# Performance work log

Hardware: AMD Instinct MI355X
Metric: run time of the kernel (lower is better)

The kernel has to match this reference:

```python
import jax, jax.numpy as jnp
import numpy as np

B, L, D, H = 64, 1024, 256, 256


def setup_inputs() -> dict:
    key = jax.random.key(0)
    ks = jax.random.split(key, 10)
    s = 0.05  # small init to keep tanh/sigmoid in linear-ish range
    return {
        "x":  jax.random.normal(ks[0], (B, L, D), jnp.float32),
        # LSTM cell params (keras gate order i, f, g, o)
        "Wk": jax.random.normal(ks[1], (D, 4 * H), jnp.float32) * s,
        "Wr": jax.random.normal(ks[2], (H, 4 * H), jnp.float32) * s,
        "b":  jnp.zeros((4 * H,), jnp.float32),
        # Attention params
        "W1": jax.random.normal(ks[3], (D, H), jnp.float32) * s,
        "b1": jnp.zeros((H,), jnp.float32),
        "W2": jax.random.normal(ks[4], (H, H), jnp.float32) * s,
        "b2": jnp.zeros((H,), jnp.float32),
        "V":  jax.random.normal(ks[5], (H, 1), jnp.float32) * s,
        "bV": jnp.zeros((1,), jnp.float32),
    }


def reference(x, Wk, Wr, b, W1, b1, W2, b2, V, bV):
    Bb, Ll, Dd = x.shape
    Hh = Wr.shape[0]
    # Encoder projection, computed once (W1 @ encoder_outputs)
    w1_e = jnp.einsum('bld,dh->blh', x, W1) + b1            # (B, L, H)
    # Decoder input is the last encoder step, repeated every step
    x_in = x[:, -1, :]                                      # (B, D)
    xz = x_in @ Wk + b                                      # (B, 4H), constant per step
    h0 = jnp.zeros((Bb, Hh), x.dtype)
    c0 = jnp.zeros((Bb, Hh), x.dtype)

    def step(carry, _):
        h, c = carry
        z = xz + h @ Wr                                     # (B, 4H)
        i, f, g, o = jnp.split(z, 4, axis=-1)
        i = jax.nn.sigmoid(i)
        f = jax.nn.sigmoid(f)
        g = jnp.tanh(g)
        o = jax.nn.sigmoid(o)
        c = f * c + i * g
        h = o * jnp.tanh(c)
        # Additive (Bahdanau) attention: v^T tanh(W1 e + W2 d)
        w2_d = (h @ W2 + b2)[:, None, :]                    # (B, 1, H)
        scores = jnp.tanh(w1_e + w2_d) @ V + bV             # (B, L, 1)
        attn = jax.nn.softmax(scores[..., 0], axis=1)       # (B, L)
        return (h, c), attn

    _, attn_seq = jax.lax.scan(step, (h0, c0), None, length=Ll)  # (L, B, L)
    return jnp.transpose(attn_seq, (1, 0, 2))               # (B, L_steps, L_ptr)
```

## Files before the change

kernel.cpp:

```cpp
#include <hip/hip_runtime.h>
#include <hip/hip_bf16.h>


#define LOG2E  1.4426950408889634f
#define C2LOG2E 2.8853900817779268f

typedef float f32x2 __attribute__((ext_vector_type(2)));

__device__ __forceinline__ unsigned f2bf(float f) {
  unsigned u = __builtin_bit_cast(unsigned, f);
  return (u + 0x7fffu + ((u >> 16) & 1u)) >> 16;
}
__device__ __forceinline__ float bfbits2f(unsigned bits) {
  return __builtin_bit_cast(float, bits << 16);
}
__device__ __forceinline__ float bfhi2f(unsigned bits) {
  return __builtin_bit_cast(float, bits & 0xffff0000u);
}

#define CHEAP_BAR()                                            \
  do {                                                         \
    asm volatile("s_waitcnt lgkmcnt(0)\n\ts_barrier" ::: "memory"); \
    __builtin_amdgcn_sched_barrier(0);                         \
  } while (0)

#if defined(__has_builtin)
#  if __has_builtin(__builtin_amdgcn_fdot2_f32_bf16)
#    define HAS_DOT2_BF16 1
#  endif
#endif

#if defined(HAS_DOT2_BF16)
typedef __bf16 bf16x2v __attribute__((ext_vector_type(2)));
__device__ __forceinline__ float dot2bf(unsigned w, unsigned h, float acc) {
  return __builtin_amdgcn_fdot2_f32_bf16(__builtin_bit_cast(bf16x2v, w),
                                         __builtin_bit_cast(bf16x2v, h), acc, false);
}
#else
__device__ __forceinline__ float dot2bf(unsigned w, unsigned h, float acc) {
  float wl = __builtin_bit_cast(float, w << 16);
  float wh = __builtin_bit_cast(float, w & 0xffff0000u);
  float hl = __builtin_bit_cast(float, h << 16);
  float hh = __builtin_bit_cast(float, h & 0xffff0000u);
  return fmaf(wh, hh, fmaf(wl, hl, acc));
}
#endif

#if defined(__has_builtin) && __has_builtin(__builtin_amdgcn_rcpf)
#  define FAST_RCP(x) __builtin_amdgcn_rcpf(x)
#else
#  define FAST_RCP(x) (1.0f / (x))
#endif

__device__ __forceinline__ float fast_sigmoid(float x) {
  return FAST_RCP(1.f + exp2f(-LOG2E * x));
}
__device__ __forceinline__ float fast_tanh(float x) {
  return 1.f - 2.f * FAST_RCP(1.f + exp2f(C2LOG2E * x));
}

__global__ __launch_bounds__(256) void k2_xz(const float* __restrict__ x,
                                             const float* __restrict__ Wk,
                                             const float* __restrict__ bvec,
                                             float* __restrict__ xz) {
  const int b = blockIdx.x, tid = threadIdx.x;
  float acc[4] = {bvec[tid], bvec[256 + tid], bvec[512 + tid], bvec[768 + tid]};
  const float* xr = x + ((size_t)b * 1024 + 1023) * 256;
  for (int d0 = 0; d0 < 256; d0 += 4) {
    const float4 xv = *(const float4*)(xr + d0);
#pragma unroll
    for (int i = 0; i < 4; ++i) {
      const float xs = (i == 0) ? xv.x : (i == 1) ? xv.y : (i == 2) ? xv.z : xv.w;
#pragma unroll
      for (int q = 0; q < 4; ++q)
        acc[q] = fmaf(xs, Wk[(size_t)(d0 + i) * 1024 + q * 256 + tid], acc[q]);
    }
  }
#pragma unroll
  for (int q = 0; q < 4; ++q) xz[b * 1024 + q * 256 + tid] = acc[q];
}

__global__
__attribute__((amdgpu_flat_work_group_size(512, 512), amdgpu_waves_per_eu(2, 2)))
void k3_fat(const float* __restrict__ xz,
            const float* __restrict__ Wr,
            unsigned short* __restrict__ hseq,
            const float* __restrict__ x,
            const float* __restrict__ W1,
            const float* __restrict__ b1,
            uint2* __restrict__ ATq) {
  __shared__ __align__(16) unsigned smem[8 * 1024 * 4 + 512 + 128];
  const int tid = threadIdx.x;
  if (blockIdx.x < 64) {
    unsigned* Wtail = smem;
    float*    z_lds = (float*)(smem + 32768);
    unsigned* h_pk  = smem + 32768 + 512;
    const int b = blockIdx.x;
    const int colA = tid, colB = tid + 512;

    unsigned wA[96], wB[96];
#pragma unroll
    for (int p = 0; p < 96; ++p) {
      wA[p] = f2bf(Wr[(size_t)(2 * p) * 1024 + colA]) |
              (f2bf(Wr[(size_t)(2 * p + 1) * 1024 + colA]) << 16);
      wB[p] = f2bf(Wr[(size_t)(2 * p) * 1024 + colB]) |
              (f2bf(Wr[(size_t)(2 * p + 1) * 1024 + colB]) << 16);
    }
#pragma unroll
    for (int gg = 0; gg < 8; ++gg) {
#pragma unroll
      for (int d = 0; d < 4; ++d) {
        const int p = 96 + gg * 4 + d;
        Wtail[(gg * 1024 + colA) * 4 + d] =
            f2bf(Wr[(size_t)(2 * p) * 1024 + colA]) |
            (f2bf(Wr[(size_t)(2 * p + 1) * 1024 + colA]) << 16);
        Wtail[(gg * 1024 + colB) * 4 + d] =
            f2bf(Wr[(size_t)(2 * p) * 1024 + colB]) |
            (f2bf(Wr[(size_t)(2 * p + 1) * 1024 + colB]) << 16);
      }
    }
    if (tid < 128) h_pk[tid] = 0u;
    const float zaA = xz[b * 1024 + colA];
    const float zaB = xz[b * 1024 + colB];
    float c = 0.f;
    CHEAP_BAR();

    for (int t = 0; t < 1024; ++t) {
      float aA0 = zaA, aA1 = 0.f, aB0 = zaB, aB1 = 0.f;
#pragma unroll
      for (int g = 0; g < 12; ++g) {
        const uint4 hp = *(const uint4*)&h_pk[4 * g];
        aA0 = dot2bf(wA[4 * g + 0], hp.x, aA0);
        aA0 = dot2bf(wA[4 * g + 1], hp.y, aA0);
        aA0 = dot2bf(wA[4 * g + 2], hp.z, aA0);
        aA0 = dot2bf(wA[4 * g + 3], hp.w, aA0);
        aB0 = dot2bf(wB[4 * g + 0], hp.x, aB0);
        aB0 = dot2bf(wB[4 * g + 1], hp.y, aB0);
        aB0 = dot2bf(wB[4 * g + 2], hp.z, aB0);
        aB0 = dot2bf(wB[4 * g + 3], hp.w, aB0);
      }
#pragma unroll
      for (int g = 12; g < 24; ++g) {
        const uint4 hp = *(const uint4*)&h_pk[4 * g];
        aA1 = dot2bf(wA[4 * g + 0], hp.x, aA1);
        aA1 = dot2bf(wA[4 * g + 1], hp.y, aA1);
        aA1 = dot2bf(wA[4 * g + 2], hp.z, aA1);
        aA1 = dot2bf(wA[4 * g + 3], hp.w, aA1);
        aB1 = dot2bf(wB[4 * g + 0], hp.x, aB1);
        aB1 = dot2bf(wB[4 * g + 1], hp.y, aB1);
        aB1 = dot2bf(wB[4 * g + 2], hp.z, aB1);
        aB1 = dot2bf(wB[4 * g + 3], hp.w, aB1);
      }
#pragma unroll
      for (int gg = 0; gg < 8; ++gg) {
        const uint4 hp = *(const uint4*)&h_pk[96 + 4 * gg];
        const uint4 wa = *(const uint4*)&Wtail[(gg * 1024 + colA) * 4];
        const uint4 wb = *(const uint4*)&Wtail[(gg * 1024 + colB) * 4];
        float& rA = (gg < 4) ? aA0 : aA1;
        float& rB = (gg < 4) ? aB0 : aB1;
        rA = dot2bf(wa.x, hp.x, rA);
        rA = dot2bf(wa.y, hp.y, rA);
        rA = dot2bf(wa.z, hp.z, rA);
        rA = dot2bf(wa.w, hp.w, rA);
        rB = dot2bf(wb.x, hp.x, rB);
        rB = dot2bf(wb.y, hp.y, rB);
        rB = dot2bf(wb.z, hp.z, rB);
        rB = dot2bf(wb.w, hp.w, rB);
      }
      const float aA = aA0 + aA1;
      const float aB = aB0 + aB1;
      if (tid >= 256) {
        z_lds[tid - 256] = aA;
        z_lds[tid]       = aB;
      }
      CHEAP_BAR();
      if (tid < 256) {
        const float zi = aA;
        const float zg = aB;
        const float zf = z_lds[tid];
        const float zo = z_lds[tid + 256];
        const float ig = fast_sigmoid(zi);
        const float fg = fast_sigmoid(zf);
        const float gv = fast_tanh(zg);
        const float og = fast_sigmoid(zo);
        c = fmaf(fg, c, ig * gv);
        const float h = og * fast_tanh(c);
        const unsigned short hb = (unsigned short)f2bf(h);
        ((unsigned short*)h_pk)[tid] = hb;
        hseq[(size_t)(t * 64 + b) * 256 + tid] = hb;
      }
      CHEAP_BAR();
    }
  } else {
    unsigned short* tile = (unsigned short*)smem;
    const int bid = blockIdx.x - 64;
    const int b  = bid >> 6;
    const int lb = bid & 63;
    const int h    = tid & 255;
    const int half = tid >> 8;
    float acc[8];
    const float bias = b1[h];
#pragma unroll
    for (int r = 0; r < 8; ++r) acc[r] = bias;
    const float* xb = x + ((size_t)(b * 1024 + lb * 16 + half * 8)) * 256;
    for (int d0 = 0; d0 < 256; d0 += 4) {
      const float w0 = W1[(d0 + 0) * 256 + h];
      const float w1 = W1[(d0 + 1) * 256 + h];
      const float w2 = W1[(d0 + 2) * 256 + h];
      const float w3 = W1[(d0 + 3) * 256 + h];
#pragma unroll
      for (int r = 0; r < 8; ++r) {
        const float4 xv = *(const float4*)(xb + r * 256 + d0);
        acc[r] = fmaf(xv.x, w0, acc[r]);
        acc[r] = fmaf(xv.y, w1, acc[r]);
        acc[r] = fmaf(xv.z, w2, acc[r]);
        acc[r] = fmaf(xv.w, w3, acc[r]);
      }
    }
#pragma unroll
    for (int r = 0; r < 8; ++r)
      tile[h * 16 + half * 8 + r] = (unsigned short)f2bf(exp2f(C2LOG2E * acc[r]));
    __syncthreads();
#pragma unroll
    for (int k = 0; k < 2; ++k) {
      const int o = k * 512 + tid;
      const int hq = o >> 4, lloc = o & 15;
      const unsigned s0 = tile[(4 * hq + 0) * 16 + lloc];
      const unsigned s1 = tile[(4 * hq + 1) * 16 + lloc];
      const unsigned s2 = tile[(4 * hq + 2) * 16 + lloc];
      const unsigned s3 = tile[(4 * hq + 3) * 16 + lloc];
      uint2 val;
      val.x = s0 | (s1 << 16);
      val.y = s2 | (s3 << 16);
      ATq[(((size_t)(b * 64 + hq)) << 10) + lb * 16 + lloc] = val;
    }
  }
}

__global__ __launch_bounds__(256) void k3b_w2d(const unsigned int* __restrict__ hseq,
                                               const float* __restrict__ W2,
                                               const float* __restrict__ b2,
                                               float* __restrict__ D) {
  const int r0 = blockIdx.x * 16;
  const int h = threadIdx.x;
  float acc[16];
  const float bias = b2[h];
#pragma unroll
  for (int r = 0; r < 16; ++r) acc[r] = bias;
  for (int m0 = 0; m0 < 128; m0 += 2) {
    const float w0 = W2[(size_t)(2 * m0 + 0) * 256 + h];
    const float w1 = W2[(size_t)(2 * m0 + 1) * 256 + h];
    const float w2 = W2[(size_t)(2 * m0 + 2) * 256 + h];
    const float w3 = W2[(size_t)(2 * m0 + 3) * 256 + h];
#pragma unroll
    for (int r = 0; r < 16; ++r) {
      const uint2 hp = *(const uint2*)&hseq[(size_t)(r0 + r) * 128 + m0];
      acc[r] = fmaf(bfbits2f(hp.x),       w0, acc[r]);
      acc[r] = fmaf(bfbits2f(hp.x >> 16), w1, acc[r]);
      acc[r] = fmaf(bfbits2f(hp.y),       w2, acc[r]);
      acc[r] = fmaf(bfbits2f(hp.y >> 16), w3, acc[r]);
    }
  }
  const int t = r0 >> 6;
  const int bb0 = r0 & 63;
#pragma unroll
  for (int r = 0; r < 16; ++r) {
    D[((size_t)(bb0 + r) * 1024 + t) * 256 + h] = exp2f(C2LOG2E * acc[r]);
  }
}

__global__ __launch_bounds__(256, 3) void k4_attn(const uint2* __restrict__ ATq,
                                                  const float* __restrict__ Dm,
                                                  const float* __restrict__ V,
                                                  float* __restrict__ out) {
  const int l  = (blockIdx.x & 7) * 512 + (blockIdx.x >> 3);
  const int b  = l >> 6;
  const int tb = l & 63;
  const int wv = threadIdx.x >> 6;
  const int lane = threadIdx.x & 63;
  const int t0 = tb * 16 + wv * 4;
  const uint2* Ab = ATq + (((size_t)b) << 16);
  const float* Db = Dm + ((size_t)(b * 1024) + t0) * 256;
  f32x2 acc2[2][16];
#pragma unroll
  for (int p = 0; p < 2; ++p)
#pragma unroll
    for (int lb = 0; lb < 16; ++lb) acc2[p][lb] = (f32x2){0.f, 0.f};

  for (int hq = 0; hq < 64; ++hq) {
    const float4 vq  = *(const float4*)(V + hq * 4);
    const float4 Dr0 = *(const float4*)(Db + 0 * 256 + hq * 4);
    const float4 Dr1 = *(const float4*)(Db + 1 * 256 + hq * 4);
    const float4 Dr2 = *(const float4*)(Db + 2 * 256 + hq * 4);
    const float4 Dr3 = *(const float4*)(Db + 3 * 256 + hq * 4);
    f32x2 Dp[2][4];
    Dp[0][0] = (f32x2){Dr0.x, Dr1.x}; Dp[0][1] = (f32x2){Dr0.y, Dr1.y};
    Dp[0][2] = (f32x2){Dr0.z, Dr1.z}; Dp[0][3] = (f32x2){Dr0.w, Dr1.w};
    Dp[1][0] = (f32x2){Dr2.x, Dr3.x}; Dp[1][1] = (f32x2){Dr2.y, Dr3.y};
    Dp[1][2] = (f32x2){Dr2.z, Dr3.z}; Dp[1][3] = (f32x2){Dr2.w, Dr3.w};
    const f32x2 v0 = (f32x2){vq.x, vq.x};
    const f32x2 v1 = (f32x2){vq.y, vq.y};
    const f32x2 v2 = (f32x2){vq.z, vq.z};
    const f32x2 v3 = (f32x2){vq.w, vq.w};
    const uint2* Ah = Ab + ((size_t)hq << 10) + lane;
#pragma unroll
    for (int lb = 0; lb < 16; ++lb) {
      const uint2 aq = Ah[lb * 64];
      const f32x2 a0 = (f32x2){bfbits2f(aq.x), bfbits2f(aq.x)};
      const f32x2 a1 = (f32x2){bfhi2f(aq.x),   bfhi2f(aq.x)};
      const f32x2 a2 = (f32x2){bfbits2f(aq.y), bfbits2f(aq.y)};
      const f32x2 a3 = (f32x2){bfhi2f(aq.y),   bfhi2f(aq.y)};
      const f32x2 one = (f32x2){1.f, 1.f};
#pragma unroll
      for (int p = 0; p < 2; ++p) {
        const f32x2 d0 = a0 * Dp[p][0] + one;
        const f32x2 d1 = a1 * Dp[p][1] + one;
        const f32x2 d2 = a2 * Dp[p][2] + one;
        const f32x2 d3 = a3 * Dp[p][3] + one;
        const f32x2 n01 = v0 * d1 + v1 * d0;
        const f32x2 n23 = v2 * d3 + v3 * d2;
        const f32x2 d01 = d0 * d1;
        const f32x2 d23 = d2 * d3;
        const f32x2 nf = n01 * d23 + n23 * d01;
        const f32x2 df = d01 * d23;
        const f32x2 r = (f32x2){FAST_RCP(df.x), FAST_RCP(df.y)};
        acc2[p][lb] += nf * r;
      }
    }
  }
#pragma unroll
  for (int p = 0; p < 2; ++p)
#pragma unroll
    for (int half = 0; half < 2; ++half) {
      const int tt = 2 * p + half;
      float s[16];
      float m = -1e30f;
#pragma unroll
      for (int lb = 0; lb < 16; ++lb) {
        s[lb] = -2.f * (half ? acc2[p][lb].y : acc2[p][lb].x);
        m = fmaxf(m, s[lb]);
      }
      for (int off = 32; off > 0; off >>= 1) m = fmaxf(m, __shfl_xor(m, off, 64));
      float pr[16];
      float sum = 0.f;
#pragma unroll
      for (int lb = 0; lb < 16; ++lb) {
        pr[lb] = exp2f((s[lb] - m) * LOG2E);
        sum += pr[lb];
      }
      for (int off = 32; off > 0; off >>= 1) sum += __shfl_xor(sum, off, 64);
      const float rs = 1.f / sum;
      float* op = out + ((size_t)(b * 1024) + (t0 + tt)) * 1024 + lane;
#pragma unroll
      for (int lb = 0; lb < 16; ++lb) op[lb * 64] = pr[lb] * rs;
    }
}

extern "C" void kernel_launch(void* const* d_in, const int* in_sizes, int n_in,
                              void* d_out, int out_size, void* d_ws, size_t ws_size,
                              hipStream_t stream) {
  (void)in_sizes; (void)n_in; (void)out_size; (void)ws_size;
  const float* x  = (const float*)d_in[0];
  const float* Wk = (const float*)d_in[1];
  const float* Wr = (const float*)d_in[2];
  const float* bb = (const float*)d_in[3];
  const float* W1 = (const float*)d_in[4];
  const float* b1 = (const float*)d_in[5];
  const float* W2 = (const float*)d_in[6];
  const float* b2 = (const float*)d_in[7];
  const float* V  = (const float*)d_in[8];

  char* ws = (char*)d_ws;
  float*          Dm   = (float*)(ws);
  uint2*          ATq  = (uint2*)(ws + 67108864);
  unsigned short* hseq = (unsigned short*)(ws + 100663296);
  float*          xz   = (float*)(ws + 134217728);
  float* out = (float*)d_out;

  hipLaunchKernelGGL(k2_xz, dim3(64), dim3(256), 0, stream, x, Wk, bb, xz);
  hipLaunchKernelGGL(k3_fat, dim3(64 + 4096), dim3(512), 0, stream,
                     xz, Wr, hseq, x, W1, b1, ATq);
  hipLaunchKernelGGL(k3b_w2d, dim3(4096), dim3(256), 0, stream,
                     (const unsigned int*)hseq, W2, b2, Dm);
  hipLaunchKernelGGL(k4_attn, dim3(4096), dim3(256), 0, stream, ATq, Dm, V, out);
}
```

Baseline: 4.374 ms.

## Widen recurrent LSTM blocks to 1024 threads, one gate column per thread

The recurrent LSTM blocks now run 1024 threads, each owning a single gate column instead of two. This halves the per-thread register-held weight slice and shortens the serial dot-product chain in each time step. The gate exchange through LDS grows to three quarters of the columns. The attention-projection blocks are also reshaped to 1024 threads with 4 rows each. In exchange, barriers now synchronise 16 waves instead of 8, and the lower register budget under 1024-thread launch bounds may cause spills of the 96-word weight array.

```diff
diff --git a/kernel.cpp b/kernel.cpp
--- a/kernel.cpp
+++ b/kernel.cpp
@@ -80,8 +80,7 @@
   for (int q = 0; q < 4; ++q) xz[b * 1024 + q * 256 + tid] = acc[q];
 }
 
-__global__
-__attribute__((amdgpu_flat_work_group_size(512, 512), amdgpu_waves_per_eu(2, 2)))
+__global__ __launch_bounds__(1024)
 void k3_fat(const float* __restrict__ xz,
             const float* __restrict__ Wr,
             unsigned short* __restrict__ hseq,
@@ -89,96 +88,72 @@
             const float* __restrict__ W1,
             const float* __restrict__ b1,
             uint2* __restrict__ ATq) {
-  __shared__ __align__(16) unsigned smem[8 * 1024 * 4 + 512 + 128];
+  __shared__ __align__(16) unsigned smem[32768 + 768 + 128];
   const int tid = threadIdx.x;
   if (blockIdx.x < 64) {
     unsigned* Wtail = smem;
     float*    z_lds = (float*)(smem + 32768);
-    unsigned* h_pk  = smem + 32768 + 512;
+    unsigned* h_pk  = smem + 32768 + 768;
     const int b = blockIdx.x;
-    const int colA = tid, colB = tid + 512;
-
-    unsigned wA[96], wB[96];
+    const int col = tid;
+
+    unsigned w[96];
 #pragma unroll
     for (int p = 0; p < 96; ++p) {
-      wA[p] = f2bf(Wr[(size_t)(2 * p) * 1024 + colA]) |
-              (f2bf(Wr[(size_t)(2 * p + 1) * 1024 + colA]) << 16);
-      wB[p] = f2bf(Wr[(size_t)(2 * p) * 1024 + colB]) |
-              (f2bf(Wr[(size_t)(2 * p + 1) * 1024 + colB]) << 16);
+      w[p] = f2bf(Wr[(size_t)(2 * p) * 1024 + col]) |
+             (f2bf(Wr[(size_t)(2 * p + 1) * 1024 + col]) << 16);
     }
 #pragma unroll
     for (int gg = 0; gg < 8; ++gg) {
 #pragma unroll
       for (int d = 0; d < 4; ++d) {
         const int p = 96 + gg * 4 + d;
-        Wtail[(gg * 1024 + colA) * 4 + d] =
-            f2bf(Wr[(size_t)(2 * p) * 1024 + colA]) |
-            (f2bf(Wr[(size_t)(2 * p + 1) * 1024 + colA]) << 16);
-        Wtail[(gg * 1024 + colB) * 4 + d] =
-            f2bf(Wr[(size_t)(2 * p) * 1024 + colB]) |
-            (f2bf(Wr[(size_t)(2 * p + 1) * 1024 + colB]) << 16);
+        Wtail[(gg * 1024 + col) * 4 + d] =
+            f2bf(Wr[(size_t)(2 * p) * 1024 + col]) |
+            (f2bf(Wr[(size_t)(2 * p + 1) * 1024 + col]) << 16);
       }
     }
     if (tid < 128) h_pk[tid] = 0u;
-    const float zaA = xz[b * 1024 + colA];
-    const float zaB = xz[b * 1024 + colB];
+    const float za = xz[b * 1024 + col];
     float c = 0.f;
     CHEAP_BAR();
 
     for (int t = 0; t < 1024; ++t) {
-      float aA0 = zaA, aA1 = 0.f, aB0 = zaB, aB1 = 0.f;
+      float a0 = za, a1 = 0.f;
 #pragma unroll
       for (int g = 0; g < 12; ++g) {
         const uint4 hp = *(const uint4*)&h_pk[4 * g];
-        aA0 = dot2bf(wA[4 * g + 0], hp.x, aA0);
-        aA0 = dot2bf(wA[4 * g + 1], hp.y, aA0);
-        aA0 = dot2bf(wA[4 * g + 2], hp.z, aA0);
-        aA0 = dot2bf(wA[4 * g + 3], hp.w, aA0);
-        aB0 = dot2bf(wB[4 * g + 0], hp.x, aB0);
-        aB0 = dot2bf(wB[4 * g + 1], hp.y, aB0);
-        aB0 = dot2bf(wB[4 * g + 2], hp.z, aB0);
-        aB0 = dot2bf(wB[4 * g + 3], hp.w, aB0);
+        a0 = dot2bf(w[4 * g + 0], hp.x, a0);
+        a0 = dot2bf(w[4 * g + 1], hp.y, a0);
+        a0 = dot2bf(w[4 * g + 2], hp.z, a0);
+        a0 = dot2bf(w[4 * g + 3], hp.w, a0);
       }
 #pragma unroll
       for (int g = 12; g < 24; ++g) {
         const uint4 hp = *(const uint4*)&h_pk[4 * g];
-        aA1 = dot2bf(wA[4 * g + 0], hp.x, aA1);
-        aA1 = dot2bf(wA[4 * g + 1], hp.y, aA1);
-        aA1 = dot2bf(wA[4 * g + 2], hp.z, aA1);
-        aA1 = dot2bf(wA[4 * g + 3], hp.w, aA1);
-        aB1 = dot2bf(wB[4 * g + 0], hp.x, aB1);
-        aB1 = dot2bf(wB[4 * g + 1], hp.y, aB1);
-        aB1 = dot2bf(wB[4 * g + 2], hp.z, aB1);
-        aB1 = dot2bf(wB[4 * g + 3], hp.w, aB1);
+        a1 = dot2bf(w[4 * g + 0], hp.x, a1);
+        a1 = dot2bf(w[4 * g + 1], hp.y, a1);
+        a1 = dot2bf(w[4 * g + 2], hp.z, a1);
+        a1 = dot2bf(w[4 * g + 3], hp.w, a1);
       }
 #pragma unroll
       for (int gg = 0; gg < 8; ++gg) {
         const uint4 hp = *(const uint4*)&h_pk[96 + 4 * gg];
-        const uint4 wa = *(const uint4*)&Wtail[(gg * 1024 + colA) * 4];
-        const uint4 wb = *(const uint4*)&Wtail[(gg * 1024 + colB) * 4];
-        float& rA = (gg < 4) ? aA0 : aA1;
-        float& rB = (gg < 4) ? aB0 : aB1;
-        rA = dot2bf(wa.x, hp.x, rA);
-        rA = dot2bf(wa.y, hp.y, rA);
-        rA = dot2bf(wa.z, hp.z, rA);
-        rA = dot2bf(wa.w, hp.w, rA);
-        rB = dot2bf(wb.x, hp.x, rB);
-        rB = dot2bf(wb.y, hp.y, rB);
-        rB = dot2bf(wb.z, hp.z, rB);
-        rB = dot2bf(wb.w, hp.w, rB);
-      }
-      const float aA = aA0 + aA1;
-      const float aB = aB0 + aB1;
-      if (tid >= 256) {
-        z_lds[tid - 256] = aA;
-        z_lds[tid]       = aB;
-      }
+        const uint4 wv = *(const uint4*)&Wtail[(gg * 1024 + col) * 4];
+        float& r = (gg < 4) ? a0 : a1;
+        r = dot2bf(wv.x, hp.x, r);
+        r = dot2bf(wv.y, hp.y, r);
+        r = dot2bf(wv.z, hp.z, r);
+        r = dot2bf(wv.w, hp.w, r);
+      }
+      const float a = a0 + a1;
+      if (tid >= 256) z_lds[tid - 256] = a;
       CHEAP_BAR();
       if (tid < 256) {
-        const float zi = aA;
-        const float zg = aB;
+        const float zi = a;
         const float zf = z_lds[tid];
-        const float zo = z_lds[tid + 256];
+        const float zg = z_lds[tid + 256];
+        const float zo = z_lds[tid + 512];
         const float ig = fast_sigmoid(zi);
         const float fg = fast_sigmoid(zf);
         const float gv = fast_tanh(zg);
@@ -196,20 +171,20 @@
     const int bid = blockIdx.x - 64;
     const int b  = bid >> 6;
     const int lb = bid & 63;
-    const int h    = tid & 255;
-    const int half = tid >> 8;
-    float acc[8];
+    const int h = tid & 255;
+    const int qr = tid >> 8;
+    float acc[4];
     const float bias = b1[h];
 #pragma unroll
-    for (int r = 0; r < 8; ++r) acc[r] = bias;
-    const float* xb = x + ((size_t)(b * 1024 + lb * 16 + half * 8)) * 256;
+    for (int r = 0; r < 4; ++r) acc[r] = bias;
+    const float* xb = x + ((size_t)(b * 1024 + lb * 16 + qr * 4)) * 256;
     for (int d0 = 0; d0 < 256; d0 += 4) {
       const float w0 = W1[(d0 + 0) * 256 + h];
       const float w1 = W1[(d0 + 1) * 256 + h];
       const float w2 = W1[(d0 + 2) * 256 + h];
       const float w3 = W1[(d0 + 3) * 256 + h];
 #pragma unroll
-      for (int r = 0; r < 8; ++r) {
+      for (int r = 0; r < 4; ++r) {
         const float4 xv = *(const float4*)(xb + r * 256 + d0);
         acc[r] = fmaf(xv.x, w0, acc[r]);
         acc[r] = fmaf(xv.y, w1, acc[r]);
@@ -218,13 +193,11 @@
       }
     }
 #pragma unroll
-    for (int r = 0; r < 8; ++r)
-      tile[h * 16 + half * 8 + r] = (unsigned short)f2bf(exp2f(C2LOG2E * acc[r]));
+    for (int r = 0; r < 4; ++r)
+      tile[h * 16 + qr * 4 + r] = (unsigned short)f2bf(exp2f(C2LOG2E * acc[r]));
     __syncthreads();
-#pragma unroll
-    for (int k = 0; k < 2; ++k) {
-      const int o = k * 512 + tid;
-      const int hq = o >> 4, lloc = o & 15;
+    {
+      const int hq = tid >> 4, lloc = tid & 15;
       const unsigned s0 = tile[(4 * hq + 0) * 16 + lloc];
       const unsigned s1 = tile[(4 * hq + 1) * 16 + lloc];
       const unsigned s2 = tile[(4 * hq + 2) * 16 + lloc];
@@ -378,7 +351,7 @@
   float* out = (float*)d_out;
 
   hipLaunchKernelGGL(k2_xz, dim3(64), dim3(256), 0, stream, x, Wk, bb, xz);
-  hipLaunchKernelGGL(k3_fat, dim3(64 + 4096), dim3(512), 0, stream,
+  hipLaunchKernelGGL(k3_fat, dim3(64 + 4096), dim3(1024), 0, stream,
                      xz, Wr, hseq, x, W1, b1, ATq);
   hipLaunchKernelGGL(k3b_w2d, dim3(4096), dim3(256), 0, stream,
                      (const unsigned int*)hseq, W2, b2, Dm);
```

After: 4.100 ms. 6.3% less time.
